# Performance work log

Hardware: AMD Instinct MI355X
Metric: run time of the kernel (lower is better)

## Reference

```python
import jax, jax.numpy as jnp
import numpy as np

N_SLOTS = 100000
D_IN = 256
D_OUT = 256
NUM_HOPS = 3


def setup_inputs() -> dict:
    key = jax.random.key(0)
    k1, k2, k3, k4, k5 = jax.random.split(key, 5)
    memory = jax.random.normal(k1, (N_SLOTS, D_IN), dtype=jnp.float32)
    query = jax.random.normal(k2, (1, D_IN), dtype=jnp.float32)
    # original init: uniform(0, 1) of shape [output_dim, input_dim]
    A = jax.random.uniform(k3, (D_OUT, D_IN), dtype=jnp.float32)
    B = jax.random.uniform(k4, (D_OUT, D_IN), dtype=jnp.float32)
    C = jax.random.uniform(k5, (D_OUT, D_IN), dtype=jnp.float32)
    return {"memory": memory, "query": query, "A": A, "B": B, "C": C}


def reference(memory, query, A, B, C):
    # Embed memory with A (addressing) and C (content), query with B.
    mem_m = memory @ A.T          # [n_slots, d_out]
    mem_c = memory @ C.T          # [n_slots, d_out]
    u = query @ B.T               # [1, d_out]
    for _ in range(NUM_HOPS):
        scores = (mem_m @ u.T).reshape(1, N_SLOTS)   # [1, n_slots]
        p = jax.nn.softmax(scores, axis=-1)          # attention over slots
        o = (p @ mem_c).reshape(1, D_OUT)            # weighted content sum
        u = o + u                                    # hop residual update
    return u
```

## Files before the change

### kernel.cpp

```cpp
#include <hip/hip_runtime.h>
#include <math.h>
#include <float.h>

#define D 256
#define NBLK 512
#define TPB 512
#define WPB (TPB / 64)

__device__ __forceinline__ float wave_reduce_sum(float s) {
    s += __shfl_xor(s, 32);
    s += __shfl_xor(s, 16);
    s += __shfl_xor(s, 8);
    s += __shfl_xor(s, 4);
    s += __shfl_xor(s, 2);
    s += __shfl_xor(s, 1);
    return s;
}
__device__ __forceinline__ float wave_reduce_max(float s) {
    s = fmaxf(s, __shfl_xor(s, 32));
    s = fmaxf(s, __shfl_xor(s, 16));
    s = fmaxf(s, __shfl_xor(s, 8));
    s = fmaxf(s, __shfl_xor(s, 4));
    s = fmaxf(s, __shfl_xor(s, 2));
    s = fmaxf(s, __shfl_xor(s, 1));
    return s;
}

__global__ __launch_bounds__(1024) void mr_init(const float* __restrict__ q,
                                                const float* __restrict__ Bm,
                                                const float* __restrict__ Am,
                                                float* __restrict__ u,
                                                float* __restrict__ v) {
    __shared__ __align__(16) float sq[D];
    __shared__ float su[D];
    __shared__ float part[4][D];
    const int tid = threadIdx.x;

    if (tid < D) sq[tid] = q[tid];
    __syncthreads();
    {
        const int j = tid >> 2, qd = tid & 3;
        const float4* Br = (const float4*)(Bm + (size_t)j * D + qd * 64);
        const float4* qr = (const float4*)(sq + qd * 64);
        float acc = 0.f;
#pragma unroll
        for (int i = 0; i < 16; ++i) {
            float4 b4 = Br[i];
            float4 q4 = qr[i];
            acc += b4.x * q4.x + b4.y * q4.y + b4.z * q4.z + b4.w * q4.w;
        }
        part[qd][j] = acc;
    }
    __syncthreads();
    if (tid < D) {
        float uu = part[0][tid] + part[1][tid] + part[2][tid] + part[3][tid];
        u[tid] = uu;
        su[tid] = uu;
    }
    __syncthreads();
    {
        const int k = tid & (D - 1), h = tid >> 8;
        const int j0 = h * 64;
        float acc = 0.f;
#pragma unroll 8
        for (int jj = 0; jj < 64; ++jj)
            acc += Am[(size_t)(j0 + jj) * D + k] * su[j0 + jj];
        part[h][k] = acc;
    }
    __syncthreads();
    if (tid < D)
        v[tid] = part[0][tid] + part[1][tid] + part[2][tid] + part[3][tid];
}

__global__ __launch_bounds__(TPB) void mr_pass(
        const float* __restrict__ mem, const float* __restrict__ v,
        float* __restrict__ wsM, float* __restrict__ wsZ,
        float* __restrict__ wsW, int nslots, int nwavesTotal) {
    const int tid  = threadIdx.x;
    const int lane = tid & 63;
    const int wid  = tid >> 6;
    const int l16  = lane & 15;
    const int g    = lane >> 4;
    const int gwave = blockIdx.x * WPB + wid;

    const int slab = (nslots + nwavesTotal - 1) / nwavesTotal;
    const int s0 = gwave * slab;
    const int s1 = min(s0 + slab, nslots);

    const float4 v0 = ((const float4*)v)[l16];
    const float4 v1 = ((const float4*)v)[l16 + 16];
    const float4 v2 = ((const float4*)v)[l16 + 32];
    const float4 v3 = ((const float4*)v)[l16 + 48];

    float m = -FLT_MAX, Z = 0.f;
    float4 w0 = {0,0,0,0}, w1 = {0,0,0,0}, w2 = {0,0,0,0}, w3 = {0,0,0,0};

    for (int base = s0; base < s1; base += 8) {
        const int slotA = base + g;
        const int slotB = base + 4 + g;
        const bool vA = slotA < s1;
        const bool vB = slotB < s1;
        const int cA = vA ? slotA : s0;
        const int cB = vB ? slotB : s0;
        const float4* rA = (const float4*)(mem + (size_t)cA * D);
        const float4* rB = (const float4*)(mem + (size_t)cB * D);
        float4 a0 = rA[l16], a1 = rA[l16 + 16], a2 = rA[l16 + 32], a3 = rA[l16 + 48];
        float4 b0 = rB[l16], b1 = rB[l16 + 16], b2 = rB[l16 + 32], b3 = rB[l16 + 48];

        float pA = a0.x*v0.x + a0.y*v0.y + a0.z*v0.z + a0.w*v0.w
                 + a1.x*v1.x + a1.y*v1.y + a1.z*v1.z + a1.w*v1.w
                 + a2.x*v2.x + a2.y*v2.y + a2.z*v2.z + a2.w*v2.w
                 + a3.x*v3.x + a3.y*v3.y + a3.z*v3.z + a3.w*v3.w;
        float pB = b0.x*v0.x + b0.y*v0.y + b0.z*v0.z + b0.w*v0.w
                 + b1.x*v1.x + b1.y*v1.y + b1.z*v1.z + b1.w*v1.w
                 + b2.x*v2.x + b2.y*v2.y + b2.z*v2.z + b2.w*v2.w
                 + b3.x*v3.x + b3.y*v3.y + b3.z*v3.z + b3.w*v3.w;
        pA += __shfl_xor(pA, 1);  pB += __shfl_xor(pB, 1);
        pA += __shfl_xor(pA, 2);  pB += __shfl_xor(pB, 2);
        pA += __shfl_xor(pA, 4);  pB += __shfl_xor(pB, 4);
        pA += __shfl_xor(pA, 8);  pB += __shfl_xor(pB, 8);

        {
            float sv = vA ? pA : -FLT_MAX;
            float mn = fmaxf(m, sv);
            float e  = vA ? __expf(sv - mn) : 0.f;
            if (__any(mn > m)) {
                float sc = __expf(m - mn);
                Z = Z * sc + e;
                w0.x = w0.x*sc + e*a0.x; w0.y = w0.y*sc + e*a0.y; w0.z = w0.z*sc + e*a0.z; w0.w = w0.w*sc + e*a0.w;
                w1.x = w1.x*sc + e*a1.x; w1.y = w1.y*sc + e*a1.y; w1.z = w1.z*sc + e*a1.z; w1.w = w1.w*sc + e*a1.w;
                w2.x = w2.x*sc + e*a2.x; w2.y = w2.y*sc + e*a2.y; w2.z = w2.z*sc + e*a2.z; w2.w = w2.w*sc + e*a2.w;
                w3.x = w3.x*sc + e*a3.x; w3.y = w3.y*sc + e*a3.y; w3.z = w3.z*sc + e*a3.z; w3.w = w3.w*sc + e*a3.w;
                m = mn;
            } else {
                Z += e;
                w0.x += e*a0.x; w0.y += e*a0.y; w0.z += e*a0.z; w0.w += e*a0.w;
                w1.x += e*a1.x; w1.y += e*a1.y; w1.z += e*a1.z; w1.w += e*a1.w;
                w2.x += e*a2.x; w2.y += e*a2.y; w2.z += e*a2.z; w2.w += e*a2.w;
                w3.x += e*a3.x; w3.y += e*a3.y; w3.z += e*a3.z; w3.w += e*a3.w;
            }
        }
        {
            float sv = vB ? pB : -FLT_MAX;
            float mn = fmaxf(m, sv);
            float e  = vB ? __expf(sv - mn) : 0.f;
            if (__any(mn > m)) {
                float sc = __expf(m - mn);
                Z = Z * sc + e;
                w0.x = w0.x*sc + e*b0.x; w0.y = w0.y*sc + e*b0.y; w0.z = w0.z*sc + e*b0.z; w0.w = w0.w*sc + e*b0.w;
                w1.x = w1.x*sc + e*b1.x; w1.y = w1.y*sc + e*b1.y; w1.z = w1.z*sc + e*b1.z; w1.w = w1.w*sc + e*b1.w;
                w2.x = w2.x*sc + e*b2.x; w2.y = w2.y*sc + e*b2.y; w2.z = w2.z*sc + e*b2.z; w2.w = w2.w*sc + e*b2.w;
                w3.x = w3.x*sc + e*b3.x; w3.y = w3.y*sc + e*b3.y; w3.z = w3.z*sc + e*b3.z; w3.w = w3.w*sc + e*b3.w;
                m = mn;
            } else {
                Z += e;
                w0.x += e*b0.x; w0.y += e*b0.y; w0.z += e*b0.z; w0.w += e*b0.w;
                w1.x += e*b1.x; w1.y += e*b1.y; w1.z += e*b1.z; w1.w += e*b1.w;
                w2.x += e*b2.x; w2.y += e*b2.y; w2.z += e*b2.z; w2.w += e*b2.w;
                w3.x += e*b3.x; w3.y += e*b3.y; w3.z += e*b3.z; w3.w += e*b3.w;
            }
        }
    }

    __shared__ __align__(16) float lw[WPB * 4][D];
    __shared__ float lm[WPB * 4];
    __shared__ float lz[WPB * 4];
    __shared__ float lf[WPB * 4];
    const int grp = wid * 4 + g;
    *(float4*)&lw[grp][(l16 +  0) * 4] = w0;
    *(float4*)&lw[grp][(l16 + 16) * 4] = w1;
    *(float4*)&lw[grp][(l16 + 32) * 4] = w2;
    *(float4*)&lw[grp][(l16 + 48) * 4] = w3;
    if (l16 == 0) { lm[grp] = m; lz[grp] = Z; }
    __syncthreads();

    if (tid < 32) {
        float mm = lm[tid];
        float M = mm;
        M = fmaxf(M, __shfl_xor(M, 1));
        M = fmaxf(M, __shfl_xor(M, 2));
        M = fmaxf(M, __shfl_xor(M, 4));
        M = fmaxf(M, __shfl_xor(M, 8));
        M = fmaxf(M, __shfl_xor(M, 16));
        float fv = __expf(mm - M);
        lf[tid] = fv;
        float zf = lz[tid] * fv;
        zf += __shfl_xor(zf, 1);
        zf += __shfl_xor(zf, 2);
        zf += __shfl_xor(zf, 4);
        zf += __shfl_xor(zf, 8);
        zf += __shfl_xor(zf, 16);
        if (tid == 0) { wsM[blockIdx.x] = M; wsZ[blockIdx.x] = zf; }
    }
    __syncthreads();

    if (tid < D) {
        float wacc = 0.f;
#pragma unroll
        for (int p = 0; p < WPB * 4; ++p) wacc += lw[p][tid] * lf[p];
        wsW[(size_t)blockIdx.x * D + tid] = wacc;
    }
}

__global__ __launch_bounds__(1024) void mr_combine(
        const float* __restrict__ wsM, const float* __restrict__ wsZ,
        const float* __restrict__ wsW, const float* __restrict__ Cm,
        const float* __restrict__ Am, float* __restrict__ u,
        float* __restrict__ v, float* __restrict__ out, int nb, int last) {
    __shared__ float f[NBLK];
    __shared__ float red[16];
    __shared__ float sMZ[2];
    __shared__ float part[4][D];
    __shared__ __align__(16) float sw[D];
    __shared__ float su[D];
    const int tid = threadIdx.x;
    const int lane = tid & 63, wv = tid >> 6;

    float lm = -FLT_MAX;
    for (int b = tid; b < nb; b += 1024) lm = fmaxf(lm, wsM[b]);
    lm = wave_reduce_max(lm);
    if (lane == 0) red[wv] = lm;
    __syncthreads();
    if (tid == 0) {
        float M = red[0];
#pragma unroll
        for (int i = 1; i < 16; ++i) M = fmaxf(M, red[i]);
        sMZ[0] = M;
    }
    __syncthreads();
    const float M = sMZ[0];

    float zp = 0.f;
    for (int b = tid; b < nb; b += 1024) {
        float fb = __expf(wsM[b] - M);
        f[b] = fb;
        zp += wsZ[b] * fb;
    }
    zp = wave_reduce_sum(zp);
    if (lane == 0) red[wv] = zp;
    __syncthreads();
    if (tid == 0) {
        float Z = 0.f;
#pragma unroll
        for (int i = 0; i < 16; ++i) Z += red[i];
        sMZ[1] = Z;
    }
    __syncthreads();
    const float Z = sMZ[1];

    {
        const int c = tid & (D - 1);
        const int chunk = tid >> 8;
        const int bpc = nb >> 2;
        const int b0 = chunk * bpc, b1 = b0 + bpc;
        float acc = 0.f;
#pragma unroll 8
        for (int b = b0; b < b1; ++b)
            acc += wsW[(size_t)b * D + c] * f[b];
        part[chunk][c] = acc;
    }
    __syncthreads();
    if (tid < D)
        sw[tid] = (part[0][tid] + part[1][tid] + part[2][tid] + part[3][tid]) / Z;
    __syncthreads();

    {
        const int j = tid >> 2, qd = tid & 3;
        const float4* Cr = (const float4*)(Cm + (size_t)j * D + qd * 64);
        const float4* wr = (const float4*)(sw + qd * 64);
        float acc = 0.f;
#pragma unroll
        for (int i = 0; i < 16; ++i) {
            float4 c4 = Cr[i];
            float4 w4 = wr[i];
            acc += c4.x * w4.x + c4.y * w4.y + c4.z * w4.z + c4.w * w4.w;
        }
        part[qd][j] = acc;
    }
    __syncthreads();
    if (tid < D) {
        float o = part[0][tid] + part[1][tid] + part[2][tid] + part[3][tid];
        float un = u[tid] + o;
        u[tid] = un;
        su[tid] = un;
        if (last) out[tid] = un;
    }
    __syncthreads();

    if (!last) {
        const int k = tid & (D - 1), h = tid >> 8;
        const int j0 = h * 64;
        float acc = 0.f;
#pragma unroll 8
        for (int jj = 0; jj < 64; ++jj)
            acc += Am[(size_t)(j0 + jj) * D + k] * su[j0 + jj];
        part[h][k] = acc;
        __syncthreads();
        if (tid < D)
            v[tid] = part[0][tid] + part[1][tid] + part[2][tid] + part[3][tid];
    }
}

extern "C" void kernel_launch(void* const* d_in, const int* in_sizes, int n_in,
                              void* d_out, int out_size, void* d_ws, size_t ws_size,
                              hipStream_t stream) {
    const float* mem = (const float*)d_in[0];
    const float* q   = (const float*)d_in[1];
    const float* A   = (const float*)d_in[2];
    const float* B   = (const float*)d_in[3];
    const float* C   = (const float*)d_in[4];
    float* out = (float*)d_out;
    float* ws  = (float*)d_ws;

    const int nslots = in_sizes[0] / D;

    long wsf = (long)(ws_size / 4);
    int nb = NBLK;
    long need = 2L * D + (long)nb * (2 + D);
    if (need > wsf) {
        nb = (int)((wsf - 2L * D) / (2 + D));
        nb &= ~3;
        if (nb < 4) nb = 4;
    }

    float* u   = ws;
    float* v   = ws + D;
    float* wsM = ws + 2 * D;
    float* wsZ = wsM + nb;
    float* wsW = wsZ + nb;

    mr_init<<<1, 1024, 0, stream>>>(q, B, A, u, v);
    for (int hop = 0; hop < 3; ++hop) {
        mr_pass<<<nb, TPB, 0, stream>>>(mem, v, wsM, wsZ, wsW,
                                        nslots, nb * WPB);
        mr_combine<<<1, 1024, 0, stream>>>(wsM, wsZ, wsW, C, A, u, v, out,
                                           nb, hop == 2 ? 1 : 0);
    }
}
```

Before: 275.1 us.

## Fuse combine into pass kernel via last-block atomic counter

Merges the single-block combine kernel into the tail of the pass kernel: each block bumps an atomic counter after a threadfence, and the last block to finish does the global softmax merge, the C projection, the residual update and the next A projection. This removes three kernel launches and their gaps. Double-buffered v arrays and per-hop counters avoid read/write races. The combine step now runs on 512 threads instead of 1024, which may lengthen that serial tail, and every block pays an extra fence and atomic.

```diff
diff --git a/kernel.cpp b/kernel.cpp
--- a/kernel.cpp
+++ b/kernel.cpp
@@ -30,12 +30,14 @@
                                                 const float* __restrict__ Bm,
                                                 const float* __restrict__ Am,
                                                 float* __restrict__ u,
-                                                float* __restrict__ v) {
+                                                float* __restrict__ v,
+                                                int* __restrict__ cnt) {
     __shared__ __align__(16) float sq[D];
     __shared__ float su[D];
     __shared__ float part[4][D];
     const int tid = threadIdx.x;
 
+    if (tid < 3) cnt[tid] = 0;
     if (tid < D) sq[tid] = q[tid];
     __syncthreads();
     {
@@ -72,10 +74,14 @@
         v[tid] = part[0][tid] + part[1][tid] + part[2][tid] + part[3][tid];
 }
 
-__global__ __launch_bounds__(TPB) void mr_pass(
-        const float* __restrict__ mem, const float* __restrict__ v,
+__global__ __launch_bounds__(TPB) void mr_pass_fused(
+        const float* __restrict__ mem, const float* __restrict__ vin,
+        float* __restrict__ vout,
         float* __restrict__ wsM, float* __restrict__ wsZ,
-        float* __restrict__ wsW, int nslots, int nwavesTotal) {
+        float* __restrict__ wsW, int* __restrict__ cnt,
+        const float* __restrict__ Cm, const float* __restrict__ Am,
+        float* __restrict__ u, float* __restrict__ out,
+        int nslots, int nwavesTotal, int nb, int last_hop) {
     const int tid  = threadIdx.x;
     const int lane = tid & 63;
     const int wid  = tid >> 6;
@@ -87,10 +93,10 @@
     const int s0 = gwave * slab;
     const int s1 = min(s0 + slab, nslots);
 
-    const float4 v0 = ((const float4*)v)[l16];
-    const float4 v1 = ((const float4*)v)[l16 + 16];
-    const float4 v2 = ((const float4*)v)[l16 + 32];
-    const float4 v3 = ((const float4*)v)[l16 + 48];
+    const float4 v0 = ((const float4*)vin)[l16];
+    const float4 v1 = ((const float4*)vin)[l16 + 16];
+    const float4 v2 = ((const float4*)vin)[l16 + 32];
+    const float4 v3 = ((const float4*)vin)[l16 + 48];
 
     float m = -FLT_MAX, Z = 0.f;
     float4 w0 = {0,0,0,0}, w1 = {0,0,0,0}, w2 = {0,0,0,0}, w3 = {0,0,0,0};
@@ -200,104 +206,107 @@
         for (int p = 0; p < WPB * 4; ++p) wacc += lw[p][tid] * lf[p];
         wsW[(size_t)blockIdx.x * D + tid] = wacc;
     }
-}
-
-__global__ __launch_bounds__(1024) void mr_combine(
-        const float* __restrict__ wsM, const float* __restrict__ wsZ,
-        const float* __restrict__ wsW, const float* __restrict__ Cm,
-        const float* __restrict__ Am, float* __restrict__ u,
-        float* __restrict__ v, float* __restrict__ out, int nb, int last) {
+
+    __shared__ int sLast;
+    __threadfence();
+    __syncthreads();
+    if (tid == 0)
+        sLast = (atomicAdd(cnt, 1) == nb - 1) ? 1 : 0;
+    __syncthreads();
+    if (!sLast) return;
+    __threadfence();
+
     __shared__ float f[NBLK];
-    __shared__ float red[16];
+    __shared__ float red[WPB];
     __shared__ float sMZ[2];
-    __shared__ float part[4][D];
+    __shared__ __align__(16) float part2[2][D];
     __shared__ __align__(16) float sw[D];
     __shared__ float su[D];
-    const int tid = threadIdx.x;
-    const int lane = tid & 63, wv = tid >> 6;
-
-    float lm = -FLT_MAX;
-    for (int b = tid; b < nb; b += 1024) lm = fmaxf(lm, wsM[b]);
-    lm = wave_reduce_max(lm);
-    if (lane == 0) red[wv] = lm;
+
+    float lmx = -FLT_MAX;
+    for (int b = tid; b < nb; b += TPB) lmx = fmaxf(lmx, wsM[b]);
+    lmx = wave_reduce_max(lmx);
+    if (lane == 0) red[wid] = lmx;
     __syncthreads();
     if (tid == 0) {
         float M = red[0];
 #pragma unroll
-        for (int i = 1; i < 16; ++i) M = fmaxf(M, red[i]);
+        for (int i = 1; i < WPB; ++i) M = fmaxf(M, red[i]);
         sMZ[0] = M;
     }
     __syncthreads();
     const float M = sMZ[0];
 
     float zp = 0.f;
-    for (int b = tid; b < nb; b += 1024) {
+    for (int b = tid; b < nb; b += TPB) {
         float fb = __expf(wsM[b] - M);
         f[b] = fb;
         zp += wsZ[b] * fb;
     }
     zp = wave_reduce_sum(zp);
-    if (lane == 0) red[wv] = zp;
+    if (lane == 0) red[wid] = zp;
     __syncthreads();
     if (tid == 0) {
-        float Z = 0.f;
-#pragma unroll
-        for (int i = 0; i < 16; ++i) Z += red[i];
-        sMZ[1] = Z;
-    }
-    __syncthreads();
-    const float Z = sMZ[1];
+        float Zs = 0.f;
+#pragma unroll
+        for (int i = 0; i < WPB; ++i) Zs += red[i];
+        sMZ[1] = Zs;
+    }
+    __syncthreads();
+    const float Zt = sMZ[1];
 
     {
         const int c = tid & (D - 1);
         const int chunk = tid >> 8;
-        const int bpc = nb >> 2;
+        const int bpc = nb >> 1;
         const int b0 = chunk * bpc, b1 = b0 + bpc;
         float acc = 0.f;
 #pragma unroll 8
         for (int b = b0; b < b1; ++b)
             acc += wsW[(size_t)b * D + c] * f[b];
-        part[chunk][c] = acc;
+        part2[chunk][c] = acc;
     }
     __syncthreads();
     if (tid < D)
-        sw[tid] = (part[0][tid] + part[1][tid] + part[2][tid] + part[3][tid]) / Z;
+        sw[tid] = (part2[0][tid] + part2[1][tid]) / Zt;
     __syncthreads();
 
     {
-        const int j = tid >> 2, qd = tid & 3;
-        const float4* Cr = (const float4*)(Cm + (size_t)j * D + qd * 64);
-        const float4* wr = (const float4*)(sw + qd * 64);
-        float acc = 0.f;
-#pragma unroll
-        for (int i = 0; i < 16; ++i) {
+        const int j = tid >> 1, h2 = tid & 1;
+        const float4* Cr = (const float4*)(Cm + (size_t)j * D + h2 * 128);
+        const float4* wr = (const float4*)(sw + h2 * 128);
+        float acc = 0.f;
+#pragma unroll
+        for (int i = 0; i < 32; ++i) {
             float4 c4 = Cr[i];
             float4 w4 = wr[i];
             acc += c4.x * w4.x + c4.y * w4.y + c4.z * w4.z + c4.w * w4.w;
         }
-        part[qd][j] = acc;
+        __syncthreads();
+        part2[h2][j] = acc;
     }
     __syncthreads();
     if (tid < D) {
-        float o = part[0][tid] + part[1][tid] + part[2][tid] + part[3][tid];
+        float o = part2[0][tid] + part2[1][tid];
         float un = u[tid] + o;
         u[tid] = un;
         su[tid] = un;
-        if (last) out[tid] = un;
-    }
-    __syncthreads();
-
-    if (!last) {
+        if (last_hop) out[tid] = un;
+    }
+    __syncthreads();
+
+    if (!last_hop) {
         const int k = tid & (D - 1), h = tid >> 8;
-        const int j0 = h * 64;
+        const int j0 = h * 128;
         float acc = 0.f;
 #pragma unroll 8
-        for (int jj = 0; jj < 64; ++jj)
+        for (int jj = 0; jj < 128; ++jj)
             acc += Am[(size_t)(j0 + jj) * D + k] * su[j0 + jj];
-        part[h][k] = acc;
+        __syncthreads();
+        part2[h][k] = acc;
         __syncthreads();
         if (tid < D)
-            v[tid] = part[0][tid] + part[1][tid] + part[2][tid] + part[3][tid];
+            vout[tid] = part2[0][tid] + part2[1][tid];
     }
 }
 
@@ -316,24 +325,30 @@
 
     long wsf = (long)(ws_size / 4);
     int nb = NBLK;
-    long need = 2L * D + (long)nb * (2 + D);
+    long fixed = 4L * D + 4;
+    long need = fixed + (long)nb * (2 + D);
     if (need > wsf) {
-        nb = (int)((wsf - 2L * D) / (2 + D));
-        nb &= ~3;
-        if (nb < 4) nb = 4;
+        nb = (int)((wsf - fixed) / (2 + D));
+        nb &= ~1;
+        if (nb < 2) nb = 2;
     }
 
     float* u   = ws;
-    float* v   = ws + D;
-    float* wsM = ws + 2 * D;
+    float* v0  = ws + D;
+    float* v1  = ws + 2 * D;
+    float* v2  = ws + 3 * D;
+    int*   cnt = (int*)(ws + 4 * D);
+    float* wsM = ws + 4 * D + 4;
     float* wsZ = wsM + nb;
     float* wsW = wsZ + nb;
 
-    mr_init<<<1, 1024, 0, stream>>>(q, B, A, u, v);
+    float* vin[3]  = {v0, v1, v2};
+    float* vout[3] = {v1, v2, v0};
+
+    mr_init<<<1, 1024, 0, stream>>>(q, B, A, u, v0, cnt);
     for (int hop = 0; hop < 3; ++hop) {
-        mr_pass<<<nb, TPB, 0, stream>>>(mem, v, wsM, wsZ, wsW,
-                                        nslots, nb * WPB);
-        mr_combine<<<1, 1024, 0, stream>>>(wsM, wsZ, wsW, C, A, u, v, out,
-                                           nb, hop == 2 ? 1 : 0);
-    }
-}
+        mr_pass_fused<<<nb, TPB, 0, stream>>>(
+            mem, vin[hop], vout[hop], wsM, wsZ, wsW, cnt + hop,
+            C, A, u, out, nslots, nb * WPB, nb, hop == 2 ? 1 : 0);
+    }
+}
```

Result: slower. 602.1 us (+118.9%).

## Split single-block combine into multi-block kernels and double pass block count

Applied to the files above, without the earlier changes.

The single-block combine kernel is replaced by three kernels. A 64-block partial reduction of the per-block weighted sums, a 4-block kernel that applies the C projection and residual, and a 4-block kernel that computes the A-projected query as four partials. The pass kernel now sums those four partials itself. The pass grid grows from 512 to 1024 blocks for more memory parallelism. This spreads the serial combine step across several CUs at the cost of extra launches per hop and more workspace traffic. Each mr_c3a block redundantly recomputes M and Z.

```diff
diff --git a/kernel.cpp b/kernel.cpp
--- a/kernel.cpp
+++ b/kernel.cpp
@@ -3,9 +3,10 @@
 #include <float.h>
 
 #define D 256
-#define NBLK 512
+#define NB 1024
 #define TPB 512
 #define WPB (TPB / 64)
+#define C2B 64
 
 __device__ __forceinline__ float wave_reduce_sum(float s) {
     s += __shfl_xor(s, 32);
@@ -30,7 +31,7 @@
                                                 const float* __restrict__ Bm,
                                                 const float* __restrict__ Am,
                                                 float* __restrict__ u,
-                                                float* __restrict__ v) {
+                                                float* __restrict__ vp0) {
     __shared__ __align__(16) float sq[D];
     __shared__ float su[D];
     __shared__ float part[4][D];
@@ -65,15 +66,12 @@
 #pragma unroll 8
         for (int jj = 0; jj < 64; ++jj)
             acc += Am[(size_t)(j0 + jj) * D + k] * su[j0 + jj];
-        part[h][k] = acc;
-    }
-    __syncthreads();
-    if (tid < D)
-        v[tid] = part[0][tid] + part[1][tid] + part[2][tid] + part[3][tid];
+        vp0[h * D + k] = acc;
+    }
 }
 
 __global__ __launch_bounds__(TPB) void mr_pass(
-        const float* __restrict__ mem, const float* __restrict__ v,
+        const float* __restrict__ mem, const float* __restrict__ vp,
         float* __restrict__ wsM, float* __restrict__ wsZ,
         float* __restrict__ wsW, int nslots, int nwavesTotal) {
     const int tid  = threadIdx.x;
@@ -87,10 +85,23 @@
     const int s0 = gwave * slab;
     const int s1 = min(s0 + slab, nslots);
 
-    const float4 v0 = ((const float4*)v)[l16];
-    const float4 v1 = ((const float4*)v)[l16 + 16];
-    const float4 v2 = ((const float4*)v)[l16 + 32];
-    const float4 v3 = ((const float4*)v)[l16 + 48];
+    const float4* vp4 = (const float4*)vp;
+    float4 v0, v1, v2, v3;
+    {
+        float4 p0, p1, p2, p3;
+#define SUM4(dst, i)                                                          \
+        p0 = vp4[(i)];        p1 = vp4[64 + (i)];                             \
+        p2 = vp4[128 + (i)];  p3 = vp4[192 + (i)];                            \
+        dst.x = p0.x + p1.x + p2.x + p3.x;                                    \
+        dst.y = p0.y + p1.y + p2.y + p3.y;                                    \
+        dst.z = p0.z + p1.z + p2.z + p3.z;                                    \
+        dst.w = p0.w + p1.w + p2.w + p3.w;
+        SUM4(v0, l16);
+        SUM4(v1, l16 + 16);
+        SUM4(v2, l16 + 32);
+        SUM4(v3, l16 + 48);
+#undef SUM4
+    }
 
     float m = -FLT_MAX, Z = 0.f;
     float4 w0 = {0,0,0,0}, w1 = {0,0,0,0}, w2 = {0,0,0,0}, w3 = {0,0,0,0};
@@ -202,70 +213,80 @@
     }
 }
 
-__global__ __launch_bounds__(1024) void mr_combine(
-        const float* __restrict__ wsM, const float* __restrict__ wsZ,
-        const float* __restrict__ wsW, const float* __restrict__ Cm,
-        const float* __restrict__ Am, float* __restrict__ u,
-        float* __restrict__ v, float* __restrict__ out, int nb, int last) {
-    __shared__ float f[NBLK];
-    __shared__ float red[16];
-    __shared__ float sMZ[2];
-    __shared__ float part[4][D];
-    __shared__ __align__(16) float sw[D];
-    __shared__ float su[D];
+__global__ __launch_bounds__(256) void mr_c2(const float* __restrict__ wsM,
+                                             const float* __restrict__ wsW,
+                                             float* __restrict__ w_part,
+                                             int nb) {
+    __shared__ float red[4];
+    __shared__ float sM;
     const int tid = threadIdx.x;
     const int lane = tid & 63, wv = tid >> 6;
 
     float lm = -FLT_MAX;
-    for (int b = tid; b < nb; b += 1024) lm = fmaxf(lm, wsM[b]);
+    for (int b = tid; b < nb; b += 256) lm = fmaxf(lm, wsM[b]);
     lm = wave_reduce_max(lm);
     if (lane == 0) red[wv] = lm;
     __syncthreads();
-    if (tid == 0) {
-        float M = red[0];
-#pragma unroll
-        for (int i = 1; i < 16; ++i) M = fmaxf(M, red[i]);
-        sMZ[0] = M;
-    }
+    if (tid == 0)
+        sM = fmaxf(fmaxf(red[0], red[1]), fmaxf(red[2], red[3]));
+    __syncthreads();
+    const float M = sM;
+
+    const int rpb = nb / C2B;
+    const int b0 = blockIdx.x * rpb;
+    float acc = 0.f;
+    for (int bb = 0; bb < rpb; ++bb) {
+        float fb = __expf(wsM[b0 + bb] - M);
+        acc += wsW[(size_t)(b0 + bb) * D + tid] * fb;
+    }
+    w_part[blockIdx.x * D + tid] = acc;
+}
+
+__global__ __launch_bounds__(256) void mr_c3a(const float* __restrict__ wsM,
+                                              const float* __restrict__ wsZ,
+                                              const float* __restrict__ w_part,
+                                              const float* __restrict__ Cm,
+                                              float* __restrict__ u,
+                                              float* __restrict__ out,
+                                              int nb, int last) {
+    __shared__ float red[4];
+    __shared__ float sMZ[2];
+    __shared__ __align__(16) float sw[D];
+    __shared__ float part[4][64];
+    const int tid = threadIdx.x;
+    const int lane = tid & 63, wv = tid >> 6;
+
+    float lm = -FLT_MAX;
+    for (int b = tid; b < nb; b += 256) lm = fmaxf(lm, wsM[b]);
+    lm = wave_reduce_max(lm);
+    if (lane == 0) red[wv] = lm;
+    __syncthreads();
+    if (tid == 0)
+        sMZ[0] = fmaxf(fmaxf(red[0], red[1]), fmaxf(red[2], red[3]));
     __syncthreads();
     const float M = sMZ[0];
 
     float zp = 0.f;
-    for (int b = tid; b < nb; b += 1024) {
-        float fb = __expf(wsM[b] - M);
-        f[b] = fb;
-        zp += wsZ[b] * fb;
-    }
+    for (int b = tid; b < nb; b += 256) zp += wsZ[b] * __expf(wsM[b] - M);
     zp = wave_reduce_sum(zp);
     if (lane == 0) red[wv] = zp;
     __syncthreads();
-    if (tid == 0) {
-        float Z = 0.f;
-#pragma unroll
-        for (int i = 0; i < 16; ++i) Z += red[i];
-        sMZ[1] = Z;
-    }
+    if (tid == 0) sMZ[1] = red[0] + red[1] + red[2] + red[3];
     __syncthreads();
     const float Z = sMZ[1];
 
     {
-        const int c = tid & (D - 1);
-        const int chunk = tid >> 8;
-        const int bpc = nb >> 2;
-        const int b0 = chunk * bpc, b1 = b0 + bpc;
         float acc = 0.f;
 #pragma unroll 8
-        for (int b = b0; b < b1; ++b)
-            acc += wsW[(size_t)b * D + c] * f[b];
-        part[chunk][c] = acc;
-    }
-    __syncthreads();
-    if (tid < D)
-        sw[tid] = (part[0][tid] + part[1][tid] + part[2][tid] + part[3][tid]) / Z;
-    __syncthreads();
-
-    {
-        const int j = tid >> 2, qd = tid & 3;
+        for (int p = 0; p < C2B; ++p)
+            acc += w_part[p * D + tid];
+        sw[tid] = acc / Z;
+    }
+    __syncthreads();
+
+    const int jloc = tid >> 2, qd = tid & 3;
+    const int j = blockIdx.x * 64 + jloc;
+    {
         const float4* Cr = (const float4*)(Cm + (size_t)j * D + qd * 64);
         const float4* wr = (const float4*)(sw + qd * 64);
         float acc = 0.f;
@@ -275,30 +296,31 @@
             float4 w4 = wr[i];
             acc += c4.x * w4.x + c4.y * w4.y + c4.z * w4.z + c4.w * w4.w;
         }
-        part[qd][j] = acc;
-    }
-    __syncthreads();
-    if (tid < D) {
+        part[qd][jloc] = acc;
+    }
+    __syncthreads();
+    if (tid < 64) {
+        const int jg = blockIdx.x * 64 + tid;
         float o = part[0][tid] + part[1][tid] + part[2][tid] + part[3][tid];
-        float un = u[tid] + o;
-        u[tid] = un;
-        su[tid] = un;
-        if (last) out[tid] = un;
-    }
-    __syncthreads();
-
-    if (!last) {
-        const int k = tid & (D - 1), h = tid >> 8;
-        const int j0 = h * 64;
-        float acc = 0.f;
+        float un = u[jg] + o;
+        u[jg] = un;
+        if (last) out[jg] = un;
+    }
+}
+
+__global__ __launch_bounds__(256) void mr_c3b(const float* __restrict__ Am,
+                                              const float* __restrict__ u,
+                                              float* __restrict__ vp_next) {
+    __shared__ float su[64];
+    const int tid = threadIdx.x;
+    const int j0 = blockIdx.x * 64;
+    if (tid < 64) su[tid] = u[j0 + tid];
+    __syncthreads();
+    float acc = 0.f;
 #pragma unroll 8
-        for (int jj = 0; jj < 64; ++jj)
-            acc += Am[(size_t)(j0 + jj) * D + k] * su[j0 + jj];
-        part[h][k] = acc;
-        __syncthreads();
-        if (tid < D)
-            v[tid] = part[0][tid] + part[1][tid] + part[2][tid] + part[3][tid];
-    }
+    for (int jj = 0; jj < 64; ++jj)
+        acc += Am[(size_t)(j0 + jj) * D + tid] * su[jj];
+    vp_next[blockIdx.x * D + tid] = acc;
 }
 
 extern "C" void kernel_launch(void* const* d_in, const int* in_sizes, int n_in,
@@ -315,25 +337,35 @@
     const int nslots = in_sizes[0] / D;
 
     long wsf = (long)(ws_size / 4);
-    int nb = NBLK;
-    long need = 2L * D + (long)nb * (2 + D);
+    int nb = NB;
+    long fixed = 256L + 3 * 4 * 256 + (long)C2B * D;
+    long need = fixed + (long)nb * (2 + D);
     if (need > wsf) {
-        nb = (int)((wsf - 2L * D) / (2 + D));
-        nb &= ~3;
-        if (nb < 4) nb = 4;
-    }
-
-    float* u   = ws;
-    float* v   = ws + D;
-    float* wsM = ws + 2 * D;
-    float* wsZ = wsM + nb;
-    float* wsW = wsZ + nb;
-
-    mr_init<<<1, 1024, 0, stream>>>(q, B, A, u, v);
+        nb = (int)((wsf - fixed) / (2 + D));
+        nb &= ~(C2B - 1);
+        if (nb < C2B) nb = C2B;
+    }
+
+    float* u      = ws;
+    float* vp0    = ws + 256;
+    float* vp1    = vp0 + 4 * 256;
+    float* vp2    = vp1 + 4 * 256;
+    float* w_part = vp2 + 4 * 256;
+    float* wsM    = w_part + C2B * D;
+    float* wsZ    = wsM + nb;
+    float* wsW    = wsZ + nb;
+
+    float* vin[3]  = {vp0, vp1, vp2};
+    float* vnx[3]  = {vp1, vp2, vp0};
+
+    mr_init<<<1, 1024, 0, stream>>>(q, B, A, u, vp0);
     for (int hop = 0; hop < 3; ++hop) {
-        mr_pass<<<nb, TPB, 0, stream>>>(mem, v, wsM, wsZ, wsW,
+        const int last = (hop == 2) ? 1 : 0;
+        mr_pass<<<nb, TPB, 0, stream>>>(mem, vin[hop], wsM, wsZ, wsW,
                                         nslots, nb * WPB);
-        mr_combine<<<1, 1024, 0, stream>>>(wsM, wsZ, wsW, C, A, u, v, out,
-                                           nb, hop == 2 ? 1 : 0);
-    }
-}
+        mr_c2<<<C2B, 256, 0, stream>>>(wsM, wsW, w_part, nb);
+        mr_c3a<<<4, 256, 0, stream>>>(wsM, wsZ, w_part, C, u, out, nb, last);
+        if (!last)
+            mr_c3b<<<4, 256, 0, stream>>>(A, u, vnx[hop]);
+    }
+}
```

New measurement: 263.7 us. 4.1% less time.
